# Kernel tuning notes

Hardware: AMD Instinct MI355X
Metric: run time of the kernel (lower is better)

## Reference

```python
import jax, jax.numpy as jnp
import numpy as np

# dims: L=seq_len, B=batch, D=n_d (hidden), PROJ=n_proj, H=heads, DEPTH=layers, V=vocab
L, B, D, PROJ, H, DEPTH, V = 1024, 4, 1024, 256, 8, 4, 32000
HD = PROJ // H          # head dim = 32
NEG = -10000.0          # additive causal mask value used by Model.set_mask


def setup_inputs() -> dict:
    key = jax.random.key(0)
    ks = jax.random.split(key, 12)
    s = (3.0 / D) ** 0.5  # init used by Model.init_weights (layer_norm-style)
    return {
        "x": jax.random.randint(ks[0], (L, B), 0, V),
        "y": jax.random.randint(ks[1], (L, B), 0, V),
        "hidden": jnp.zeros((DEPTH, B, D), jnp.float32),            # init_hidden
        "emb_W": jax.random.uniform(ks[2], (V, D), jnp.float32, -s, s),
        # SRU++ attention transform per layer: q-proj, kv-proj, output to 3*D (U matrices)
        "W1": jax.random.normal(ks[3], (DEPTH, D, PROJ), jnp.float32) / np.float32(np.sqrt(D)),
        "W2": jax.random.normal(ks[4], (DEPTH, PROJ, 2 * PROJ), jnp.float32) / np.float32(np.sqrt(PROJ)),
        "W3": jax.random.normal(ks[5], (DEPTH, PROJ, 3 * D), jnp.float32) / np.float32(np.sqrt(PROJ)),
        "alpha": jax.random.normal(ks[6], (DEPTH,), jnp.float32) * 0.1,  # rezero scalar (nonzero so attn path is live)
        "weight_c": jax.random.normal(ks[7], (DEPTH, 2 * D), jnp.float32) * 0.1,  # (v_f, v_r)
        # bias = (b_f, b_r); forget bias initialized to highway_bias = -3
        "bias": jnp.concatenate([jnp.full((DEPTH, D), -3.0, jnp.float32), jnp.zeros((DEPTH, D), jnp.float32)], axis=-1),
        "Wout": jax.random.uniform(ks[8], (D, V), jnp.float32, -s, s),
        "bout": jnp.zeros((V,), jnp.float32),
    }


def _attention_transform(h, W1, W2, W3, alpha, mask):
    # SRUppAttention (no memory, no layer_norm, dropout=0)
    z = jnp.einsum('lbd,dp->lbp', h, W1)                 # (L,B,PROJ) query / residual
    kv = jnp.einsum('lbp,pq->lbq', z, W2)                # (L,B,2*PROJ)
    k, v = jnp.split(kv, 2, axis=-1)
    q = z.reshape(L, B, H, HD) * (HD ** -0.5)
    k = k.reshape(L, B, H, HD)
    v = v.reshape(L, B, H, HD)
    scores = jnp.einsum('lbhd,sbhd->bhls', q, k) + mask  # causal additive mask
    attn = jax.nn.softmax(scores, axis=-1)
    out = jnp.einsum('bhls,sbhd->lbhd', attn, v).reshape(L, B, PROJ)
    out = out * alpha + z                                # rezero residual
    return jnp.einsum('lbp,pk->lbk', out, W3)            # U: (L,B,3*D)


def _sru_recurrence(U, residual, c0, vf, vr, bf, br):
    # SRU elementwise highway recurrence (k=3, identity activation, no rescale)
    u = U.reshape(L, B, D, 3)
    u0 = u[..., 0]
    u1 = u[..., 1] + bf
    u2 = u[..., 2] + br

    def step(c, xs):
        u0t, u1t, u2t, rt = xs                           # each (B,D)
        f = jax.nn.sigmoid(u1t + vf * c)
        c = f * c + (1.0 - f) * u0t
        r = jax.nn.sigmoid(u2t + vr * c)
        h = r * c + (1.0 - r) * rt                       # highway on layer input
        return c, h

    c_last, hs = jax.lax.scan(step, c0, (u0, u1, u2, residual))
    return hs, c_last


def reference(x, y, hidden, emb_W, W1, W2, W3, alpha, weight_c, bias, Wout, bout):
    mask = jnp.triu(jnp.full((L, L), NEG, jnp.float32), 1)   # Model.set_mask, mem_len=0
    h = emb_W[x]                                             # (L,B,D) embedding lookup
    for i in range(DEPTH):
        U = _attention_transform(h, W1[i], W2[i], W3[i], alpha[i], mask)
        h, _ = _sru_recurrence(U, h, hidden[i],
                               weight_c[i, :D], weight_c[i, D:],
                               bias[i, :D], bias[i, D:])
    logits = jnp.einsum('lbd,dv->lbv', h, Wout) + bout       # (L,B,V)
    logp = jax.nn.log_softmax(logits, axis=-1)
    loss = -jnp.take_along_axis(logp, y[..., None], axis=-1)[..., 0]  # (L,B) per-token CE
    return loss
```

## Files before the change

kernel.cpp:

```cpp
#include <hip/hip_runtime.h>
#include <hip/hip_bf16.h>
#include <stdint.h>

#define L_ 1024
#define B_ 4
#define D_ 1024
#define PROJ_ 256
#define H_ 8
#define V_ 32000
#define M_ 4096

typedef __bf16 bf16x8 __attribute__((ext_vector_type(8)));
typedef float f32x4 __attribute__((ext_vector_type(4)));

#define AS3(p) ((__attribute__((address_space(3))) void*)(p))
#define AS1(p) ((const __attribute__((address_space(1))) void*)(p))

__global__ __launch_bounds__(256) void k_embed(const int* __restrict__ x,
                                               const float* __restrict__ emb,
                                               __hip_bfloat16* __restrict__ h) {
  int gid = blockIdx.x * 256 + threadIdx.x;
  int row = gid >> 8;
  int d0 = (gid & 255) << 2;
  int tok = x[row];
  const float4 v = *(const float4*)(emb + (size_t)tok * D_ + d0);
  union { __hip_bfloat16 o[4]; uint2 u; } cv;
  cv.o[0] = __float2bfloat16(v.x);
  cv.o[1] = __float2bfloat16(v.y);
  cv.o[2] = __float2bfloat16(v.z);
  cv.o[3] = __float2bfloat16(v.w);
  *(uint2*)(h + (size_t)row * D_ + d0) = cv.u;
}

__global__ __launch_bounds__(256) void k_transpose(const float* __restrict__ in,
                                                   __hip_bfloat16* __restrict__ out,
                                                   int K, int N,
                                                   long in_stride, long out_stride,
                                                   int perm3) {
  __shared__ float t[64][65];
  in += (size_t)blockIdx.z * in_stride;
  out += (size_t)blockIdx.z * out_stride;
  int n0 = blockIdx.x * 64, k0 = blockIdx.y * 64;
  int r = threadIdx.x >> 4, c4 = (threadIdx.x & 15) << 2;
#pragma unroll
  for (int p = 0; p < 4; p++) {
    float4 v = *(const float4*)(in + (size_t)(k0 + p * 16 + r) * N + n0 + c4);
    t[p * 16 + r][c4 + 0] = v.x;
    t[p * 16 + r][c4 + 1] = v.y;
    t[p * 16 + r][c4 + 2] = v.z;
    t[p * 16 + r][c4 + 3] = v.w;
  }
  __syncthreads();
  int n = threadIdx.x >> 2, kg = (threadIdx.x & 3) << 4;
  union { __hip_bfloat16 b[16]; uint4 u[2]; } cv;
#pragma unroll
  for (int i = 0; i < 16; i++) cv.b[i] = __float2bfloat16(t[kg + i][n]);
  int nn = n0 + n;
  if (perm3) nn = (nn % 3) * D_ + nn / 3;
  uint4* op = (uint4*)(out + (size_t)nn * K + k0 + kg);
  op[0] = cv.u[0];
  op[1] = cv.u[1];
}

template <bool CLS>
__global__ __launch_bounds__(256) void k_gemm_bt(
    const __hip_bfloat16* __restrict__ A, const __hip_bfloat16* __restrict__ Bt,
    __hip_bfloat16* __restrict__ C, int K, int N,
    const float* __restrict__ bout, const int* __restrict__ y,
    float2* __restrict__ lse, float* __restrict__ logitY) {
  __shared__ __hip_bfloat16 As[128 * 64];
  __shared__ __hip_bfloat16 Bs[128 * 64];
  const int tid = threadIdx.x;
  const int lane = tid & 63, wave = tid >> 6;
  const int quad = lane >> 4, l16 = lane & 15;
  const int wm = wave & 1, wn = wave >> 1;
  const int row0 = blockIdx.x * 128, col0 = blockIdx.y * 128;

  f32x4 acc[4][4] = {};

  const __hip_bfloat16* Abase = A + (size_t)row0 * K;
  const __hip_bfloat16* Bbase = Bt + (size_t)col0 * K;
  const int m_s = tid >> 3;
  const int ko_sw = (((tid & 7) ^ (m_s & 7)) << 3);
  const int xr = l16 & 7;

  for (int k0 = 0; k0 < K; k0 += 64) {
    __syncthreads();
#pragma unroll
    for (int call = 0; call < 4; call++) {
      int m = m_s + call * 32;
      __builtin_amdgcn_global_load_lds(AS1(Abase + (size_t)m * K + k0 + ko_sw),
                                       AS3(As + (call * 256 + wave * 64) * 8),
                                       16, 0, 0);
      __builtin_amdgcn_global_load_lds(AS1(Bbase + (size_t)m * K + k0 + ko_sw),
                                       AS3(Bs + (call * 256 + wave * 64) * 8),
                                       16, 0, 0);
    }
    __syncthreads();
#pragma unroll
    for (int kk = 0; kk < 2; kk++) {
      bf16x8 af[4], bfr[4];
#pragma unroll
      for (int mi = 0; mi < 4; mi++)
        af[mi] = *(const bf16x8*)(As + (wm * 64 + mi * 16 + l16) * 64 +
                                  (((kk * 4 + quad) ^ xr) << 3));
#pragma unroll
      for (int ni = 0; ni < 4; ni++)
        bfr[ni] = *(const bf16x8*)(Bs + (wn * 64 + ni * 16 + l16) * 64 +
                                   (((kk * 4 + quad) ^ xr) << 3));
#pragma unroll
      for (int mi = 0; mi < 4; mi++)
#pragma unroll
        for (int ni = 0; ni < 4; ni++)
          acc[mi][ni] = __builtin_amdgcn_mfma_f32_16x16x32_bf16(af[mi], bfr[ni],
                                                                acc[mi][ni], 0, 0, 0);
    }
  }

  if constexpr (!CLS) {
#pragma unroll
    for (int mi = 0; mi < 4; mi++)
#pragma unroll
      for (int ni = 0; ni < 4; ni++)
#pragma unroll
        for (int r = 0; r < 4; r++) {
          int row = row0 + wm * 64 + mi * 16 + quad * 4 + r;
          int col = col0 + wn * 64 + ni * 16 + l16;
          C[(size_t)row * N + col] = __float2bfloat16(acc[mi][ni][r]);
        }
  } else {
    const int chunk = blockIdx.y * 2 + wn;
    float bv[4];
#pragma unroll
    for (int ni = 0; ni < 4; ni++)
      bv[ni] = bout[col0 + wn * 64 + ni * 16 + l16];
#pragma unroll
    for (int mi = 0; mi < 4; mi++) {
#pragma unroll
      for (int r = 0; r < 4; r++) {
        int row = row0 + wm * 64 + mi * 16 + quad * 4 + r;
        float v0 = acc[mi][0][r] + bv[0];
        float v1 = acc[mi][1][r] + bv[1];
        float v2 = acc[mi][2][r] + bv[2];
        float v3 = acc[mi][3][r] + bv[3];
        int yv = y[row];
        int cb = col0 + wn * 64 + l16;
        if (yv == cb + 0)  logitY[row] = v0;
        if (yv == cb + 16) logitY[row] = v1;
        if (yv == cb + 32) logitY[row] = v2;
        if (yv == cb + 48) logitY[row] = v3;
        float m = fmaxf(fmaxf(v0, v1), fmaxf(v2, v3));
#pragma unroll
        for (int off = 1; off < 16; off <<= 1)
          m = fmaxf(m, __shfl_xor(m, off, 64));
        float s = __expf(v0 - m) + __expf(v1 - m) + __expf(v2 - m) + __expf(v3 - m);
#pragma unroll
        for (int off = 1; off < 16; off <<= 1)
          s += __shfl_xor(s, off, 64);
        if (l16 == 0)
          lse[(size_t)chunk * M_ + row] = make_float2(m, s);
      }
    }
  }
}

__global__ __launch_bounds__(512, 2) void k_gemm_cls256(
    const __hip_bfloat16* __restrict__ A, const __hip_bfloat16* __restrict__ Bt,
    int K, const float* __restrict__ bout, const int* __restrict__ y,
    float2* __restrict__ lse, float* __restrict__ logitY) {
  __shared__ __align__(16) __hip_bfloat16 As[2][16384];
  __shared__ __align__(16) __hip_bfloat16 Bs[2][16384];
  const int tid = threadIdx.x;
  const int lane = tid & 63, wave = tid >> 6;
  const int quad = lane >> 4, l16 = lane & 15;
  const int wm = wave >> 2, wn = wave & 3;

  const int bid = blockIdx.y * 16 + blockIdx.x;
  const int swzb = (bid & 7) * 250 + (bid >> 3);
  const int bx = swzb & 15, by = swzb >> 4;
  const int row0 = bx * 256, col0 = by * 256;

  const int m_l = wave * 8 + (lane >> 3);
  const int sw = ((lane & 7) ^ (lane >> 3)) << 3;
  const __hip_bfloat16* Ag = A + (size_t)(row0 + m_l) * K + sw;
  const __hip_bfloat16* Bg = Bt + (size_t)(col0 + m_l) * K + sw;

#define STAGE_A(buf, r, ko)                                                   \
  __builtin_amdgcn_global_load_lds(AS1(Ag + (size_t)(r) * 64 * K + (ko)),     \
                                   AS3(&As[buf][((r) * 64 + wave * 8) * 64]), \
                                   16, 0, 0)
#define STAGE_B(buf, r, ko)                                                   \
  __builtin_amdgcn_global_load_lds(AS1(Bg + (size_t)(r) * 64 * K + (ko)),     \
                                   AS3(&Bs[buf][((r) * 64 + wave * 8) * 64]), \
                                   16, 0, 0)

  const int aoff = (wm * 128 + l16) * 64;
  const int boff = (wn * 64 + l16) * 64;
  const int cc0 = ((quad) ^ (l16 & 7)) << 3;
  const int cc1 = ((4 + quad) ^ (l16 & 7)) << 3;

  f32x4 acc[8][4] = {};
  bf16x8 a4[4], b0[4], b1[4];

#define DS_B(buf, breg, cck)                                                  \
  do {                                                                        \
    _Pragma("unroll") for (int ni = 0; ni < 4; ++ni)                          \
        breg[ni] = *(const bf16x8*)(&Bs[buf][boff + ni * 1024 + (cck)]);      \
  } while (0)

#define DS_A(buf, mlo, cck)                                                   \
  do {                                                                        \
    _Pragma("unroll") for (int mi = 0; mi < 4; ++mi)                          \
        a4[mi] = *(const bf16x8*)(&As[buf][aoff + ((mlo) + mi) * 1024 + (cck)]); \
  } while (0)

#define MFMA_Q(mlo, breg)                                                     \
  do {                                                                        \
    __builtin_amdgcn_s_barrier();                                             \
    asm volatile("s_waitcnt lgkmcnt(0)" ::: "memory");                        \
    __builtin_amdgcn_sched_barrier(0);                                        \
    __builtin_amdgcn_s_setprio(1);                                            \
    _Pragma("unroll") for (int mi = 0; mi < 4; ++mi)                          \
        _Pragma("unroll") for (int ni = 0; ni < 4; ++ni)                      \
            acc[(mlo) + mi][ni] = __builtin_amdgcn_mfma_f32_16x16x32_bf16(    \
                a4[mi], breg[ni], acc[(mlo) + mi][ni], 0, 0, 0);              \
    __builtin_amdgcn_s_setprio(0);                                            \
  } while (0)

#define BAR() __builtin_amdgcn_s_barrier()

  STAGE_A(0, 0, 0); STAGE_A(0, 1, 0); STAGE_A(0, 2, 0); STAGE_A(0, 3, 0);
  STAGE_B(0, 0, 0); STAGE_B(0, 1, 0); STAGE_B(0, 2, 0); STAGE_B(0, 3, 0);
  STAGE_B(1, 0, 64); STAGE_B(1, 1, 64); STAGE_B(1, 2, 64); STAGE_B(1, 3, 64);
  asm volatile("s_waitcnt vmcnt(4)" ::: "memory");
  BAR();

  for (int i = 0; i < 7; ++i) {
    const size_t kT1 = (size_t)i * 128 + 64;
    const size_t kN0 = (size_t)i * 128 + 128;
    const size_t kN1 = (size_t)i * 128 + 192;
    DS_B(0, b0, cc0); DS_A(0, 0, cc0);
    STAGE_A(1, 0, kT1); STAGE_A(1, 1, kT1); STAGE_A(1, 2, kT1); STAGE_A(1, 3, kT1);
    MFMA_Q(0, b0); BAR();
    DS_B(0, b1, cc1); DS_A(0, 0, cc1);
    MFMA_Q(0, b1); BAR();
    DS_A(0, 4, cc0);
    STAGE_B(0, 0, kN0); STAGE_B(0, 1, kN0);
    MFMA_Q(4, b0); BAR();
    DS_A(0, 4, cc1);
    STAGE_B(0, 2, kN0); STAGE_B(0, 3, kN0);
    MFMA_Q(4, b1);
    asm volatile("s_waitcnt vmcnt(4)" ::: "memory");
    BAR();
    DS_B(1, b0, cc0); DS_A(1, 0, cc0);
    STAGE_A(0, 0, kN0); STAGE_A(0, 1, kN0); STAGE_A(0, 2, kN0); STAGE_A(0, 3, kN0);
    MFMA_Q(0, b0); BAR();
    DS_B(1, b1, cc1); DS_A(1, 0, cc1);
    MFMA_Q(0, b1); BAR();
    DS_A(1, 4, cc0);
    STAGE_B(1, 0, kN1); STAGE_B(1, 1, kN1);
    MFMA_Q(4, b0); BAR();
    DS_A(1, 4, cc1);
    STAGE_B(1, 2, kN1); STAGE_B(1, 3, kN1);
    MFMA_Q(4, b1);
    asm volatile("s_waitcnt vmcnt(4)" ::: "memory");
    BAR();
  }
  {
    const size_t kT1 = (size_t)7 * 128 + 64;
    DS_B(0, b0, cc0); DS_A(0, 0, cc0);
    STAGE_A(1, 0, kT1); STAGE_A(1, 1, kT1); STAGE_A(1, 2, kT1); STAGE_A(1, 3, kT1);
    MFMA_Q(0, b0); BAR();
    DS_B(0, b1, cc1); DS_A(0, 0, cc1);
    MFMA_Q(0, b1); BAR();
    DS_A(0, 4, cc0);
    MFMA_Q(4, b0); BAR();
    DS_A(0, 4, cc1);
    MFMA_Q(4, b1);
    asm volatile("s_waitcnt vmcnt(0)" ::: "memory");
    BAR();
    DS_B(1, b0, cc0); DS_A(1, 0, cc0);
    MFMA_Q(0, b0); BAR();
    DS_B(1, b1, cc1); DS_A(1, 0, cc1);
    MFMA_Q(0, b1); BAR();
    DS_A(1, 4, cc0);
    MFMA_Q(4, b0); BAR();
    DS_A(1, 4, cc1);
    MFMA_Q(4, b1);
  }

  const int chunk = by * 4 + wn;
  float bv[4];
#pragma unroll
  for (int ni = 0; ni < 4; ++ni)
    bv[ni] = bout[col0 + wn * 64 + ni * 16 + l16];
#pragma unroll
  for (int mi = 0; mi < 8; ++mi) {
#pragma unroll
    for (int r = 0; r < 4; ++r) {
      int row = row0 + wm * 128 + mi * 16 + quad * 4 + r;
      float v0 = acc[mi][0][r] + bv[0];
      float v1 = acc[mi][1][r] + bv[1];
      float v2 = acc[mi][2][r] + bv[2];
      float v3 = acc[mi][3][r] + bv[3];
      int yv = y[row];
      int cb = col0 + wn * 64 + l16;
      if (yv == cb + 0)  logitY[row] = v0;
      if (yv == cb + 16) logitY[row] = v1;
      if (yv == cb + 32) logitY[row] = v2;
      if (yv == cb + 48) logitY[row] = v3;
      float m = fmaxf(fmaxf(v0, v1), fmaxf(v2, v3));
#pragma unroll
      for (int off = 1; off < 16; off <<= 1)
        m = fmaxf(m, __shfl_xor(m, off, 64));
      float s = __expf(v0 - m) + __expf(v1 - m) + __expf(v2 - m) + __expf(v3 - m);
#pragma unroll
      for (int off = 1; off < 16; off <<= 1)
        s += __shfl_xor(s, off, 64);
      if (l16 == 0)
        lse[(size_t)chunk * M_ + row] = make_float2(m, s);
    }
  }
#undef STAGE_A
#undef STAGE_B
#undef DS_A
#undef DS_B
#undef MFMA_Q
#undef BAR
}

__global__ __launch_bounds__(256) void k_gemm_cls_f32(
    const __hip_bfloat16* __restrict__ A, const float* __restrict__ B,
    int K, int N, const float* __restrict__ bout, const int* __restrict__ y,
    float2* __restrict__ lse, float* __restrict__ logitY) {
  __shared__ __hip_bfloat16 As[128 * 40];
  __shared__ __hip_bfloat16 Bs[128 * 40];
  const int tid = threadIdx.x;
  const int lane = tid & 63, wave = tid >> 6;
  const int quad = lane >> 4, l16 = lane & 15;
  const int wm = wave & 1, wn = wave >> 1;
  const int row0 = blockIdx.x * 128, col0 = blockIdx.y * 128;
  f32x4 acc[4][4] = {};
  const int a_m = tid >> 1, a_k = (tid & 1) << 4;
  const int b_k = tid >> 3, b_n = (tid & 7) << 4;
  for (int k0 = 0; k0 < K; k0 += 32) {
    const uint4* ap = (const uint4*)(A + (size_t)(row0 + a_m) * K + k0 + a_k);
    uint4 av0 = ap[0];
    uint4 av1 = ap[1];
    const float* bp = B + (size_t)(k0 + b_k) * N + col0 + b_n;
    float4 bv0 = *(const float4*)(bp + 0);
    float4 bv1 = *(const float4*)(bp + 4);
    float4 bv2 = *(const float4*)(bp + 8);
    float4 bv3 = *(const float4*)(bp + 12);
    __syncthreads();
    *(uint4*)(As + a_m * 40 + a_k) = av0;
    *(uint4*)(As + a_m * 40 + a_k + 8) = av1;
    {
      float tmp[16] = {bv0.x, bv0.y, bv0.z, bv0.w, bv1.x, bv1.y, bv1.z, bv1.w,
                       bv2.x, bv2.y, bv2.z, bv2.w, bv3.x, bv3.y, bv3.z, bv3.w};
#pragma unroll
      for (int j = 0; j < 16; j++)
        Bs[(b_n + j) * 40 + b_k] = __float2bfloat16(tmp[j]);
    }
    __syncthreads();
    bf16x8 af[4], bfr[4];
#pragma unroll
    for (int mi = 0; mi < 4; mi++)
      af[mi] = *(const bf16x8*)(As + (wm * 64 + mi * 16 + l16) * 40 + quad * 8);
#pragma unroll
    for (int ni = 0; ni < 4; ni++)
      bfr[ni] = *(const bf16x8*)(Bs + (wn * 64 + ni * 16 + l16) * 40 + quad * 8);
#pragma unroll
    for (int mi = 0; mi < 4; mi++)
#pragma unroll
      for (int ni = 0; ni < 4; ni++)
        acc[mi][ni] = __builtin_amdgcn_mfma_f32_16x16x32_bf16(af[mi], bfr[ni],
                                                              acc[mi][ni], 0, 0, 0);
  }
  const int chunk = blockIdx.y * 2 + wn;
  float bv[4];
#pragma unroll
  for (int ni = 0; ni < 4; ni++)
    bv[ni] = bout[col0 + wn * 64 + ni * 16 + l16];
#pragma unroll
  for (int mi = 0; mi < 4; mi++) {
#pragma unroll
    for (int r = 0; r < 4; r++) {
      int row = row0 + wm * 64 + mi * 16 + quad * 4 + r;
      float v0 = acc[mi][0][r] + bv[0];
      float v1 = acc[mi][1][r] + bv[1];
      float v2 = acc[mi][2][r] + bv[2];
      float v3 = acc[mi][3][r] + bv[3];
      int yv = y[row];
      int cb = col0 + wn * 64 + l16;
      if (yv == cb + 0)  logitY[row] = v0;
      if (yv == cb + 16) logitY[row] = v1;
      if (yv == cb + 32) logitY[row] = v2;
      if (yv == cb + 48) logitY[row] = v3;
      float m = fmaxf(fmaxf(v0, v1), fmaxf(v2, v3));
#pragma unroll
      for (int off = 1; off < 16; off <<= 1)
        m = fmaxf(m, __shfl_xor(m, off, 64));
      float s = __expf(v0 - m) + __expf(v1 - m) + __expf(v2 - m) + __expf(v3 - m);
#pragma unroll
      for (int off = 1; off < 16; off <<= 1)
        s += __shfl_xor(s, off, 64);
      if (l16 == 0)
        lse[(size_t)chunk * M_ + row] = make_float2(m, s);
    }
  }
}

__global__ __launch_bounds__(256) void k_attn_mfma(
    const __hip_bfloat16* __restrict__ z, const __hip_bfloat16* __restrict__ kv,
    __hip_bfloat16* __restrict__ ao, const float* __restrict__ alpha_p) {
  __shared__ __hip_bfloat16 Qs[64 * 40];
  __shared__ __hip_bfloat16 Ks[128 * 40];
  __shared__ __hip_bfloat16 Vt[32 * 136];
  __shared__ __hip_bfloat16 Ps[64 * 136];
  const int tid = threadIdx.x;
  const int lane = tid & 63, wave = tid >> 6;
  const int quad = lane >> 4, l16 = lane & 15;
  const int bh = blockIdx.y, b = bh >> 3, h = bh & 7;
  const int q0 = blockIdx.x * 64;
  const float scale = 0.17677669529663687f;

  {
    int r = tid >> 2, c = (tid & 3) << 3;
    *(uint4*)(Qs + r * 40 + c) =
        *(const uint4*)(z + ((size_t)(q0 + r) * B_ + b) * PROJ_ + h * 32 + c);
  }

  float m_i[4] = {-1e30f, -1e30f, -1e30f, -1e30f};
  float l_i[4] = {0.f, 0.f, 0.f, 0.f};
  f32x4 o_acc[2] = {};

  const int ntile = (q0 + 191) >> 7;

  for (int t = 0; t < ntile; t++) {
    const int s0 = t << 7;
    __syncthreads();
    {
      int r = tid >> 1, c = (tid & 1) << 4;
      const uint4* kp =
          (const uint4*)(kv + ((size_t)(s0 + r) * B_ + b) * 512 + h * 32 + c);
      *(uint4*)(Ks + r * 40 + c) = kp[0];
      *(uint4*)(Ks + r * 40 + c + 8) = kp[1];
    }
    {
      int s = tid >> 1, dbase = (tid & 1) << 4;
      const __hip_bfloat16* vp =
          kv + ((size_t)(s0 + s) * B_ + b) * 512 + 256 + h * 32 + dbase;
      union { uint4 u; __hip_bfloat16 e[8]; } t0, t1;
      t0.u = *(const uint4*)vp;
      t1.u = *(const uint4*)(vp + 8);
#pragma unroll
      for (int j = 0; j < 8; j++) {
        Vt[(dbase + j) * 136 + s] = t0.e[j];
        Vt[(dbase + 8 + j) * 136 + s] = t1.e[j];
      }
    }
    __syncthreads();

    f32x4 sacc[8] = {};
    {
      bf16x8 aq = *(const bf16x8*)(Qs + (wave * 16 + l16) * 40 + quad * 8);
#pragma unroll
      for (int ni = 0; ni < 8; ni++) {
        bf16x8 bk = *(const bf16x8*)(Ks + (ni * 16 + l16) * 40 + quad * 8);
        sacc[ni] = __builtin_amdgcn_mfma_f32_16x16x32_bf16(aq, bk, sacc[ni], 0, 0, 0);
      }
    }

#pragma unroll
    for (int r = 0; r < 4; r++) {
      const int qrow = q0 + wave * 16 + quad * 4 + r;
      float mx = -1e30f;
#pragma unroll
      for (int ni = 0; ni < 8; ni++) {
        int s = s0 + ni * 16 + l16;
        float v = (s <= qrow) ? sacc[ni][r] * scale : -1e30f;
        sacc[ni][r] = v;
        mx = fmaxf(mx, v);
      }
#pragma unroll
      for (int off = 1; off < 16; off <<= 1)
        mx = fmaxf(mx, __shfl_xor(mx, off, 64));
      float mnew = fmaxf(m_i[r], mx);
      float al = __expf(m_i[r] - mnew);
      m_i[r] = mnew;
      float ps = 0.f;
#pragma unroll
      for (int ni = 0; ni < 8; ni++) {
        float p = __expf(sacc[ni][r] - mnew);
        Ps[(wave * 16 + quad * 4 + r) * 136 + ni * 16 + l16] = __float2bfloat16(p);
        ps += p;
      }
#pragma unroll
      for (int off = 1; off < 16; off <<= 1)
        ps += __shfl_xor(ps, off, 64);
      l_i[r] = l_i[r] * al + ps;
      o_acc[0][r] *= al;
      o_acc[1][r] *= al;
    }

#pragma unroll
    for (int ks = 0; ks < 4; ks++) {
      bf16x8 ap = *(const bf16x8*)(Ps + (wave * 16 + l16) * 136 + ks * 32 + quad * 8);
#pragma unroll
      for (int ni = 0; ni < 2; ni++) {
        bf16x8 bv = *(const bf16x8*)(Vt + (ni * 16 + l16) * 136 + ks * 32 + quad * 8);
        o_acc[ni] = __builtin_amdgcn_mfma_f32_16x16x32_bf16(ap, bv, o_acc[ni], 0, 0, 0);
      }
    }
  }

  const float arz = alpha_p[0];
#pragma unroll
  for (int ni = 0; ni < 2; ni++)
#pragma unroll
    for (int r = 0; r < 4; r++) {
      int row = q0 + wave * 16 + quad * 4 + r;
      size_t oi = ((size_t)row * B_ + b) * PROJ_ + h * 32 + ni * 16 + l16;
      float res = __bfloat162float(z[oi]);
      ao[oi] = __float2bfloat16(o_acc[ni][r] / l_i[r] * arz + res);
    }
}

__global__ __launch_bounds__(64) void k_sru(const __hip_bfloat16* __restrict__ U,
                                            __hip_bfloat16* __restrict__ h,
                                            const float* __restrict__ hidden,
                                            const float* __restrict__ wc,
                                            const float* __restrict__ bias) {
  int tid = blockIdx.x * 64 + threadIdx.x;
  int b = tid >> 10, d = tid & 1023;
  float vf = wc[d], vr = wc[D_ + d];
  float bfs = bias[d], brs = bias[D_ + d];
  float c = hidden[b * D_ + d];
  const int US = B_ * 3 * D_, HS = B_ * D_;
  const __hip_bfloat16* up = U + (size_t)b * 3 * D_ + d;
  __hip_bfloat16* hp = h + (size_t)b * D_ + d;

#define SRU_LOAD(u0a, u1a, u2a, rsa, base_l)                                  \
  do {                                                                        \
    _Pragma("unroll") for (int j = 0; j < 8; j++) {                           \
      size_t o = (size_t)((base_l) + j) * US;                                 \
      u0a[j] = __bfloat162float(up[o]);                                       \
      u1a[j] = __bfloat162float(up[o + D_]);                                  \
      u2a[j] = __bfloat162float(up[o + 2 * D_]);                              \
      rsa[j] = __bfloat162float(hp[(size_t)((base_l) + j) * HS]);             \
    }                                                                         \
  } while (0)

#define SRU_COMP(u0a, u1a, u2a, rsa, base_l)                                  \
  do {                                                                        \
    _Pragma("unroll") for (int j = 0; j < 8; j++) {                           \
      float f = __builtin_amdgcn_rcpf(1.f + __expf(-(u1a[j] + bfs + vf * c)));\
      c = u0a[j] + f * (c - u0a[j]);                                          \
      float r = __builtin_amdgcn_rcpf(1.f + __expf(-(u2a[j] + brs + vr * c)));\
      hp[(size_t)((base_l) + j) * HS] =                                       \
          __float2bfloat16(rsa[j] + r * (c - rsa[j]));                        \
    }                                                                         \
  } while (0)

  float a0[8], a1[8], a2[8], ar[8];
  float c0[8], c1[8], c2[8], cr[8];
  SRU_LOAD(a0, a1, a2, ar, 0);
  for (int l0 = 0; l0 < L_; l0 += 16) {
    SRU_LOAD(c0, c1, c2, cr, l0 + 8);
    SRU_COMP(a0, a1, a2, ar, l0);
    if (l0 + 16 < L_) SRU_LOAD(a0, a1, a2, ar, l0 + 16);
    SRU_COMP(c0, c1, c2, cr, l0 + 8);
  }
#undef SRU_LOAD
#undef SRU_COMP
}

__global__ __launch_bounds__(256) void k_finalize(const float2* __restrict__ lse,
                                                  const float* __restrict__ logitY,
                                                  float* __restrict__ out) {
  int row = blockIdx.x * 256 + threadIdx.x;
  float M = -1e30f, S = 0.f;
  for (int c = 0; c < V_ / 64; c++) {
    float2 p = lse[(size_t)c * M_ + row];
    if (p.x > M) {
      S = S * __expf(M - p.x) + p.y;
      M = p.x;
    } else {
      S += p.y * __expf(p.x - M);
    }
  }
  out[row] = M + logf(S) - logitY[row];
}

extern "C" void kernel_launch(void* const* d_in, const int* in_sizes, int n_in,
                              void* d_out, int out_size, void* d_ws, size_t ws_size,
                              hipStream_t stream) {
  const int* x = (const int*)d_in[0];
  const int* y = (const int*)d_in[1];
  const float* hidden = (const float*)d_in[2];
  const float* emb = (const float*)d_in[3];
  const float* W1 = (const float*)d_in[4];
  const float* W2 = (const float*)d_in[5];
  const float* W3 = (const float*)d_in[6];
  const float* alpha = (const float*)d_in[7];
  const float* wc = (const float*)d_in[8];
  const float* bias = (const float*)d_in[9];
  const float* Wout = (const float*)d_in[10];
  const float* bout = (const float*)d_in[11];

  char* ws = (char*)d_ws;
  __hip_bfloat16* h16  = (__hip_bfloat16*)(ws + 0);
  __hip_bfloat16* z16  = (__hip_bfloat16*)(ws + 8388608);
  __hip_bfloat16* kv16 = (__hip_bfloat16*)(ws + 10485760);
  __hip_bfloat16* ao16 = (__hip_bfloat16*)(ws + 14680064);
  __hip_bfloat16* W1t  = (__hip_bfloat16*)(ws + 16777216);
  __hip_bfloat16* W2t  = (__hip_bfloat16*)(ws + 18874368);
  __hip_bfloat16* W3t  = (__hip_bfloat16*)(ws + 19922944);
  __hip_bfloat16* U16  = (__hip_bfloat16*)(ws + 26214400);
  const bool fast = ws_size >= 109723648ull;
  __hip_bfloat16* Woutt = (__hip_bfloat16*)(ws + 26214400);
  float2* lse    = (float2*)(ws + (fast ? 93323264u : 26214400u));
  float* logitY  = (float*)(ws + (fast ? 109707264u : 42598400u));
  float* out     = (float*)d_out;

  k_embed<<<4096, 256, 0, stream>>>(x, emb, h16);
  k_transpose<<<dim3(4, 16, 4), 256, 0, stream>>>(W1, W1t, D_, PROJ_,
                                                  (long)D_ * PROJ_, (long)PROJ_ * D_, 0);
  k_transpose<<<dim3(8, 4, 4), 256, 0, stream>>>(W2, W2t, PROJ_, 2 * PROJ_,
                                                 (long)PROJ_ * 2 * PROJ_,
                                                 (long)2 * PROJ_ * PROJ_, 0);
  k_transpose<<<dim3(48, 4, 4), 256, 0, stream>>>(W3, W3t, PROJ_, 3 * D_,
                                                  (long)PROJ_ * 3 * D_,
                                                  (long)3 * D_ * PROJ_, 1);
  for (int i = 0; i < 4; i++) {
    k_gemm_bt<false><<<dim3(32, 2), 256, 0, stream>>>(
        h16, W1t + (size_t)i * PROJ_ * D_, z16, D_, PROJ_,
        nullptr, nullptr, nullptr, nullptr);
    k_gemm_bt<false><<<dim3(32, 4), 256, 0, stream>>>(
        z16, W2t + (size_t)i * 2 * PROJ_ * PROJ_, kv16, PROJ_, 2 * PROJ_,
        nullptr, nullptr, nullptr, nullptr);
    k_attn_mfma<<<dim3(16, 32), 256, 0, stream>>>(z16, kv16, ao16, alpha + i);
    k_gemm_bt<false><<<dim3(32, 24), 256, 0, stream>>>(
        ao16, W3t + (size_t)i * 3 * D_ * PROJ_, U16, PROJ_, 3 * D_,
        nullptr, nullptr, nullptr, nullptr);
    k_sru<<<64, 64, 0, stream>>>(U16, h16, hidden + (size_t)i * B_ * D_,
                                 wc + (size_t)i * 2 * D_, bias + (size_t)i * 2 * D_);
  }
  if (fast) {
    k_transpose<<<dim3(500, 16, 1), 256, 0, stream>>>(Wout, Woutt, D_, V_, 0, 0, 0);
    k_gemm_cls256<<<dim3(16, 125), 512, 0, stream>>>(h16, Woutt, D_, bout, y,
                                                     lse, logitY);
  } else {
    k_gemm_cls_f32<<<dim3(32, V_ / 128), 256, 0, stream>>>(
        h16, Wout, D_, V_, bout, y, lse, logitY);
  }
  k_finalize<<<16, 256, 0, stream>>>(lse, logitY, out);
}
```

Before: 1.496 ms.

## Run vocabulary classifier GEMM in FP8 instead of BF16

Converts the transposed output weight matrix and the final hidden states to FP8 (e4m3) and runs the 4096x32000x1024 classifier GEMM with FP8 MFMA instructions, halving bytes staged through LDS and global memory per tile. The staging and swizzle layout is rewritten for byte elements, with half as many global-to-LDS loads per stage. A separate conversion kernel for the activations is added. The lower precision of both operands risks a noticeably less accurate loss.

```diff
diff --git a/kernel.cpp b/kernel.cpp
--- a/kernel.cpp
+++ b/kernel.cpp
@@ -62,6 +62,51 @@
   op[1] = cv.u[1];
 }
 
+__global__ __launch_bounds__(256) void k_transpose8(const float* __restrict__ in,
+                                                    unsigned char* __restrict__ out) {
+  __shared__ float t[64][65];
+  int n0 = blockIdx.x * 64, k0 = blockIdx.y * 64;
+  int r = threadIdx.x >> 4, c4 = (threadIdx.x & 15) << 2;
+#pragma unroll
+  for (int p = 0; p < 4; p++) {
+    float4 v = *(const float4*)(in + (size_t)(k0 + p * 16 + r) * V_ + n0 + c4);
+    t[p * 16 + r][c4 + 0] = v.x;
+    t[p * 16 + r][c4 + 1] = v.y;
+    t[p * 16 + r][c4 + 2] = v.z;
+    t[p * 16 + r][c4 + 3] = v.w;
+  }
+  __syncthreads();
+  int n = threadIdx.x >> 2, kg = (threadIdx.x & 3) << 4;
+  uint4 w;
+  int* wp = (int*)&w;
+#pragma unroll
+  for (int g = 0; g < 4; g++) {
+    int v = __builtin_amdgcn_cvt_pk_fp8_f32(t[kg + g * 4 + 0][n], t[kg + g * 4 + 1][n], 0, false);
+    v = __builtin_amdgcn_cvt_pk_fp8_f32(t[kg + g * 4 + 2][n], t[kg + g * 4 + 3][n], v, true);
+    wp[g] = v;
+  }
+  *(uint4*)(out + (size_t)(n0 + n) * 1024 + k0 + kg) = w;
+}
+
+__global__ __launch_bounds__(256) void k_to_fp8(const __hip_bfloat16* __restrict__ in,
+                                                unsigned char* __restrict__ out) {
+  int gid = blockIdx.x * 256 + threadIdx.x;
+  union { uint4 u; unsigned short s[8]; } v;
+  v.u = *(const uint4*)(in + (size_t)gid * 8);
+  float f[8];
+#pragma unroll
+  for (int j = 0; j < 8; j++) f[j] = __uint_as_float((unsigned)v.s[j] << 16);
+  uint2 w;
+  int* wp = (int*)&w;
+#pragma unroll
+  for (int g = 0; g < 2; g++) {
+    int p = __builtin_amdgcn_cvt_pk_fp8_f32(f[g * 4 + 0], f[g * 4 + 1], 0, false);
+    p = __builtin_amdgcn_cvt_pk_fp8_f32(f[g * 4 + 2], f[g * 4 + 3], p, true);
+    wp[g] = p;
+  }
+  *(uint2*)(out + (size_t)gid * 8) = w;
+}
+
 template <bool CLS>
 __global__ __launch_bounds__(256) void k_gemm_bt(
     const __hip_bfloat16* __restrict__ A, const __hip_bfloat16* __restrict__ Bt,
@@ -164,12 +209,12 @@
   }
 }
 
-__global__ __launch_bounds__(512, 2) void k_gemm_cls256(
-    const __hip_bfloat16* __restrict__ A, const __hip_bfloat16* __restrict__ Bt,
-    int K, const float* __restrict__ bout, const int* __restrict__ y,
+__global__ __launch_bounds__(512, 2) void k_gemm_cls256f8(
+    const unsigned char* __restrict__ A8, const unsigned char* __restrict__ Bt8,
+    const float* __restrict__ bout, const int* __restrict__ y,
     float2* __restrict__ lse, float* __restrict__ logitY) {
-  __shared__ __align__(16) __hip_bfloat16 As[2][16384];
-  __shared__ __align__(16) __hip_bfloat16 Bs[2][16384];
+  __shared__ __align__(16) unsigned char As8[2][16384];
+  __shared__ __align__(16) unsigned char Bs8[2][16384];
   const int tid = threadIdx.x;
   const int lane = tid & 63, wave = tid >> 6;
   const int quad = lane >> 4, l16 = lane & 15;
@@ -180,59 +225,60 @@
   const int bx = swzb & 15, by = swzb >> 4;
   const int row0 = bx * 256, col0 = by * 256;
 
-  const int m_l = wave * 8 + (lane >> 3);
-  const int sw = ((lane & 7) ^ (lane >> 3)) << 3;
-  const __hip_bfloat16* Ag = A + (size_t)(row0 + m_l) * K + sw;
-  const __hip_bfloat16* Bg = Bt + (size_t)(col0 + m_l) * K + sw;
-
-#define STAGE_A(buf, r, ko)                                                   \
-  __builtin_amdgcn_global_load_lds(AS1(Ag + (size_t)(r) * 64 * K + (ko)),     \
-                                   AS3(&As[buf][((r) * 64 + wave * 8) * 64]), \
+  const int m8_l = wave * 16 + (lane >> 2);
+  const int sw8 = (((lane & 3) ^ ((lane >> 2) & 3)) << 4);
+  const unsigned char* Ag = A8 + (size_t)(row0 + m8_l) * 1024 + sw8;
+  const unsigned char* Bg = Bt8 + (size_t)(col0 + m8_l) * 1024 + sw8;
+
+#define STAGE_A(buf, r, ko)                                                    \
+  __builtin_amdgcn_global_load_lds(AS1(Ag + (size_t)(r) * 131072 + (ko)),      \
+                                   AS3(&As8[buf][(r) * 8192 + wave * 1024]),   \
                                    16, 0, 0)
-#define STAGE_B(buf, r, ko)                                                   \
-  __builtin_amdgcn_global_load_lds(AS1(Bg + (size_t)(r) * 64 * K + (ko)),     \
-                                   AS3(&Bs[buf][((r) * 64 + wave * 8) * 64]), \
+#define STAGE_B(buf, r, ko)                                                    \
+  __builtin_amdgcn_global_load_lds(AS1(Bg + (size_t)(r) * 131072 + (ko)),      \
+                                   AS3(&Bs8[buf][(r) * 8192 + wave * 1024]),   \
                                    16, 0, 0)
 
-  const int aoff = (wm * 128 + l16) * 64;
-  const int boff = (wn * 64 + l16) * 64;
-  const int cc0 = ((quad) ^ (l16 & 7)) << 3;
-  const int cc1 = ((4 + quad) ^ (l16 & 7)) << 3;
+  const int x3 = l16 & 3;
+  const int aoff8 = (wm * 128 + l16) * 64;
+  const int boff8 = (wn * 64 + l16) * 64;
+  const int cc0 = ((((quad >> 1) + 0) ^ x3) << 4) | ((quad & 1) << 3);
+  const int cc1 = ((((quad >> 1) + 2) ^ x3) << 4) | ((quad & 1) << 3);
 
   f32x4 acc[8][4] = {};
-  bf16x8 a4[4], b0[4], b1[4];
-
-#define DS_B(buf, breg, cck)                                                  \
-  do {                                                                        \
-    _Pragma("unroll") for (int ni = 0; ni < 4; ++ni)                          \
-        breg[ni] = *(const bf16x8*)(&Bs[buf][boff + ni * 1024 + (cck)]);      \
+  long a4[4], b0[4], b1[4];
+
+#define DS_B(buf, breg, cck)                                                   \
+  do {                                                                         \
+    _Pragma("unroll") for (int ni = 0; ni < 4; ++ni)                           \
+        breg[ni] = *(const long*)(&Bs8[buf][boff8 + ni * 1024 + (cck)]);       \
   } while (0)
 
-#define DS_A(buf, mlo, cck)                                                   \
-  do {                                                                        \
-    _Pragma("unroll") for (int mi = 0; mi < 4; ++mi)                          \
-        a4[mi] = *(const bf16x8*)(&As[buf][aoff + ((mlo) + mi) * 1024 + (cck)]); \
+#define DS_A(buf, mlo, cck)                                                    \
+  do {                                                                         \
+    _Pragma("unroll") for (int mi = 0; mi < 4; ++mi)                           \
+        a4[mi] = *(const long*)(&As8[buf][aoff8 + ((mlo) + mi) * 1024 + (cck)]); \
   } while (0)
 
-#define MFMA_Q(mlo, breg)                                                     \
-  do {                                                                        \
-    __builtin_amdgcn_s_barrier();                                             \
-    asm volatile("s_waitcnt lgkmcnt(0)" ::: "memory");                        \
-    __builtin_amdgcn_sched_barrier(0);                                        \
-    __builtin_amdgcn_s_setprio(1);                                            \
-    _Pragma("unroll") for (int mi = 0; mi < 4; ++mi)                          \
-        _Pragma("unroll") for (int ni = 0; ni < 4; ++ni)                      \
-            acc[(mlo) + mi][ni] = __builtin_amdgcn_mfma_f32_16x16x32_bf16(    \
-                a4[mi], breg[ni], acc[(mlo) + mi][ni], 0, 0, 0);              \
-    __builtin_amdgcn_s_setprio(0);                                            \
+#define MFMA_Q(mlo, breg)                                                      \
+  do {                                                                         \
+    __builtin_amdgcn_s_barrier();                                              \
+    asm volatile("s_waitcnt lgkmcnt(0)" ::: "memory");                         \
+    __builtin_amdgcn_sched_barrier(0);                                         \
+    __builtin_amdgcn_s_setprio(1);                                             \
+    _Pragma("unroll") for (int mi = 0; mi < 4; ++mi)                           \
+        _Pragma("unroll") for (int ni = 0; ni < 4; ++ni)                       \
+            acc[(mlo) + mi][ni] = __builtin_amdgcn_mfma_f32_16x16x32_fp8_fp8(  \
+                a4[mi], breg[ni], acc[(mlo) + mi][ni], 0, 0, 0);               \
+    __builtin_amdgcn_s_setprio(0);                                             \
   } while (0)
 
 #define BAR() __builtin_amdgcn_s_barrier()
 
-  STAGE_A(0, 0, 0); STAGE_A(0, 1, 0); STAGE_A(0, 2, 0); STAGE_A(0, 3, 0);
-  STAGE_B(0, 0, 0); STAGE_B(0, 1, 0); STAGE_B(0, 2, 0); STAGE_B(0, 3, 0);
-  STAGE_B(1, 0, 64); STAGE_B(1, 1, 64); STAGE_B(1, 2, 64); STAGE_B(1, 3, 64);
-  asm volatile("s_waitcnt vmcnt(4)" ::: "memory");
+  STAGE_A(0, 0, 0); STAGE_A(0, 1, 0);
+  STAGE_B(0, 0, 0); STAGE_B(0, 1, 0);
+  STAGE_B(1, 0, 64); STAGE_B(1, 1, 64);
+  asm volatile("s_waitcnt vmcnt(2)" ::: "memory");
   BAR();
 
   for (int i = 0; i < 7; ++i) {
@@ -240,36 +286,36 @@
     const size_t kN0 = (size_t)i * 128 + 128;
     const size_t kN1 = (size_t)i * 128 + 192;
     DS_B(0, b0, cc0); DS_A(0, 0, cc0);
-    STAGE_A(1, 0, kT1); STAGE_A(1, 1, kT1); STAGE_A(1, 2, kT1); STAGE_A(1, 3, kT1);
+    STAGE_A(1, 0, kT1); STAGE_A(1, 1, kT1);
     MFMA_Q(0, b0); BAR();
     DS_B(0, b1, cc1); DS_A(0, 0, cc1);
     MFMA_Q(0, b1); BAR();
     DS_A(0, 4, cc0);
-    STAGE_B(0, 0, kN0); STAGE_B(0, 1, kN0);
+    STAGE_B(0, 0, kN0);
     MFMA_Q(4, b0); BAR();
     DS_A(0, 4, cc1);
-    STAGE_B(0, 2, kN0); STAGE_B(0, 3, kN0);
+    STAGE_B(0, 1, kN0);
     MFMA_Q(4, b1);
-    asm volatile("s_waitcnt vmcnt(4)" ::: "memory");
+    asm volatile("s_waitcnt vmcnt(2)" ::: "memory");
     BAR();
     DS_B(1, b0, cc0); DS_A(1, 0, cc0);
-    STAGE_A(0, 0, kN0); STAGE_A(0, 1, kN0); STAGE_A(0, 2, kN0); STAGE_A(0, 3, kN0);
+    STAGE_A(0, 0, kN0); STAGE_A(0, 1, kN0);
     MFMA_Q(0, b0); BAR();
     DS_B(1, b1, cc1); DS_A(1, 0, cc1);
     MFMA_Q(0, b1); BAR();
     DS_A(1, 4, cc0);
-    STAGE_B(1, 0, kN1); STAGE_B(1, 1, kN1);
+    STAGE_B(1, 0, kN1);
     MFMA_Q(4, b0); BAR();
     DS_A(1, 4, cc1);
-    STAGE_B(1, 2, kN1); STAGE_B(1, 3, kN1);
+    STAGE_B(1, 1, kN1);
     MFMA_Q(4, b1);
-    asm volatile("s_waitcnt vmcnt(4)" ::: "memory");
+    asm volatile("s_waitcnt vmcnt(2)" ::: "memory");
     BAR();
   }
   {
     const size_t kT1 = (size_t)7 * 128 + 64;
     DS_B(0, b0, cc0); DS_A(0, 0, cc0);
-    STAGE_A(1, 0, kT1); STAGE_A(1, 1, kT1); STAGE_A(1, 2, kT1); STAGE_A(1, 3, kT1);
+    STAGE_A(1, 0, kT1); STAGE_A(1, 1, kT1);
     MFMA_Q(0, b0); BAR();
     DS_B(0, b1, cc1); DS_A(0, 0, cc1);
     MFMA_Q(0, b1); BAR();
@@ -619,7 +665,8 @@
   __hip_bfloat16* W3t  = (__hip_bfloat16*)(ws + 19922944);
   __hip_bfloat16* U16  = (__hip_bfloat16*)(ws + 26214400);
   const bool fast = ws_size >= 109723648ull;
-  __hip_bfloat16* Woutt = (__hip_bfloat16*)(ws + 26214400);
+  unsigned char* Woutt8 = (unsigned char*)(ws + 26214400);
+  unsigned char* A8     = (unsigned char*)(ws + 59768832);
   float2* lse    = (float2*)(ws + (fast ? 93323264u : 26214400u));
   float* logitY  = (float*)(ws + (fast ? 109707264u : 42598400u));
   float* out     = (float*)d_out;
@@ -648,9 +695,10 @@
                                  wc + (size_t)i * 2 * D_, bias + (size_t)i * 2 * D_);
   }
   if (fast) {
-    k_transpose<<<dim3(500, 16, 1), 256, 0, stream>>>(Wout, Woutt, D_, V_, 0, 0, 0);
-    k_gemm_cls256<<<dim3(16, 125), 512, 0, stream>>>(h16, Woutt, D_, bout, y,
-                                                     lse, logitY);
+    k_transpose8<<<dim3(500, 16), 256, 0, stream>>>(Wout, Woutt8);
+    k_to_fp8<<<2048, 256, 0, stream>>>(h16, A8);
+    k_gemm_cls256f8<<<dim3(16, 125), 512, 0, stream>>>(A8, Woutt8, bout, y,
+                                                       lse, logitY);
   } else {
     k_gemm_cls_f32<<<dim3(32, V_ / 128), 256, 0, stream>>>(
         h16, Wout, D_, V_, bout, y, lse, logitY);
```

Result: slower. 1.568 ms (+4.8%).
